# Performance work log

Hardware: AMD Instinct MI355X
Metric: run time of the kernel (lower is better)

Reference implementation:

```python
import jax, jax.numpy as jnp
import numpy as np

B, N, H, O = 262144, 64, 256, 64
MAX_ITER = 30
TOL = 1e-7
NU = 1.0


def setup_inputs() -> dict:
    key = jax.random.key(0)
    kx, kr, k1, k2, k3, k4 = jax.random.split(key, 6)
    x = jax.random.normal(kx, (B, N), dtype=jnp.float32) * 3.0
    r = jax.random.uniform(kr, (N,), dtype=jnp.float32) + 0.5  # positive rates in [0.5, 1.5)
    # MLP params (torch Linear: y = x @ W.T + b), Kaiming-ish scaling
    W1 = jax.random.normal(k1, (H, N), dtype=jnp.float32) * (1.0 / np.sqrt(N))
    b1 = jax.random.normal(k2, (H,), dtype=jnp.float32) * 0.01
    W2 = jax.random.normal(k3, (O, H), dtype=jnp.float32) * (1.0 / np.sqrt(H))
    b2 = jax.random.normal(k4, (O,), dtype=jnp.float32) * 0.01
    return {"x": x, "r": r, "W1": W1, "b1": b1, "W2": W2, "b2": b2}


def _solve_s(x, r):
    """Vectorized Newton solve of sum_i e^{-2 r_i s} x_i^2 = 1 per sample.

    Replicates solve_s_single: s starts at 0, up to MAX_ITER Newton steps,
    frozen once |F(s)| < TOL; all-zero samples return s = 0.
    """
    x2 = x * x  # [B, N]
    zero_mask = jnp.all(jnp.abs(x) <= 1e-12, axis=1)  # torch.allclose(x, 0, atol=1e-12)

    def body(_, s):
        e = jnp.exp(-2.0 * r[None, :] * s[:, None])        # [B, N]
        val = jnp.sum(e * x2, axis=1) - 1.0                # F(s)     [B]
        dval = jnp.sum(-2.0 * r[None, :] * e * x2, axis=1) # F'(s)    [B]
        safe_d = jnp.where(dval == 0.0, 1.0, dval)
        step = val / safe_d
        step = jnp.where((jnp.abs(val) < TOL) | zero_mask, 0.0, step)
        return s - step

    s0 = jnp.zeros(x.shape[0], dtype=x.dtype)
    return jax.lax.fori_loop(0, MAX_ITER, body, s0)


def reference(x, r, W1, b1, W2, b2):
    S = _solve_s(x, r)[:, None]                 # [B, 1], detached in torch (built via .item())
    S = jax.lax.stop_gradient(S)
    x_sphere = x * jnp.exp(-r[None, :] * S)     # d(-s) x
    h = jnp.maximum(x_sphere @ W1.T + b1, 0.0)  # [B, H]
    mlp_out = h @ W2.T + b2                     # [B, O]
    return mlp_out * jnp.exp(NU * S)
```

## Files before the change

### kernel.cpp

```cpp
#include <hip/hip_runtime.h>

typedef __attribute__((ext_vector_type(8))) short short8;
typedef __attribute__((ext_vector_type(4))) float floatx4;

static __device__ __forceinline__ unsigned short f2bf(float f) {
    unsigned u = __float_as_uint(f);
    u += 0x7FFFu + ((u >> 16) & 1u);
    return (unsigned short)(u >> 16);
}

__global__ __launch_bounds__(512, 2) void fused_k(const float* __restrict__ x,
                                                  const float* __restrict__ r,
                                                  const float* __restrict__ W1f,
                                                  const float* __restrict__ b1,
                                                  const float* __restrict__ W2f,
                                                  const float* __restrict__ b2,
                                                  float* __restrict__ out,
                                                  int tiles_per_block) {
    __shared__ unsigned short sW1[256 * 64];
    __shared__ unsigned short sW2[64 * 256];
    __shared__ unsigned short sH[128 * 32];

    int tid = threadIdx.x;

    const float4* w1f4 = (const float4*)W1f;
#pragma unroll
    for (int c = 0; c < 4; ++c) {
        int g = tid + c * 512;
        float4 lo = w1f4[2 * g], hi = w1f4[2 * g + 1];
        uint4 p;
        p.x = (unsigned)f2bf(lo.x) | ((unsigned)f2bf(lo.y) << 16);
        p.y = (unsigned)f2bf(lo.z) | ((unsigned)f2bf(lo.w) << 16);
        p.z = (unsigned)f2bf(hi.x) | ((unsigned)f2bf(hi.y) << 16);
        p.w = (unsigned)f2bf(hi.z) | ((unsigned)f2bf(hi.w) << 16);
        int row = g >> 3, ch = g & 7;
        *(uint4*)&sW1[row * 64 + (ch ^ (row & 7)) * 8] = p;
    }
    const float4* w2f4 = (const float4*)W2f;
#pragma unroll
    for (int c = 0; c < 4; ++c) {
        int g = tid + c * 512;
        float4 lo = w2f4[2 * g], hi = w2f4[2 * g + 1];
        uint4 p;
        p.x = (unsigned)f2bf(lo.x) | ((unsigned)f2bf(lo.y) << 16);
        p.y = (unsigned)f2bf(lo.z) | ((unsigned)f2bf(lo.w) << 16);
        p.z = (unsigned)f2bf(hi.x) | ((unsigned)f2bf(hi.y) << 16);
        p.w = (unsigned)f2bf(hi.z) | ((unsigned)f2bf(hi.w) << 16);
        int row = g >> 5, ch = g & 31;
        *(uint4*)&sW2[row * 256 + (ch ^ (row & 7)) * 8] = p;
    }
    __syncthreads();

    int wave = tid >> 6, lane = tid & 63;
    int q = lane >> 4, l16 = lane & 15;
    int sx = l16 & 7;

    float bias1[16];
#pragma unroll
    for (int n = 0; n < 16; ++n) bias1[n] = b1[n * 16 + l16];
    float bias2[4];
#pragma unroll
    for (int n = 0; n < 4; ++n) bias2[n] = b2[n * 16 + l16];

    const float L2E2 = 2.8853900817779268f;
    float rl2[16];
    {
        const float4* r4 = (const float4*)r;
        float4 ra = r4[2 * q], rb = r4[2 * q + 1];
        float4 rc = r4[8 + 2 * q], rd = r4[8 + 2 * q + 1];
        rl2[0] = ra.x * L2E2; rl2[1] = ra.y * L2E2; rl2[2] = ra.z * L2E2; rl2[3] = ra.w * L2E2;
        rl2[4] = rb.x * L2E2; rl2[5] = rb.y * L2E2; rl2[6] = rb.z * L2E2; rl2[7] = rb.w * L2E2;
        rl2[8] = rc.x * L2E2; rl2[9] = rc.y * L2E2; rl2[10] = rc.z * L2E2; rl2[11] = rc.w * L2E2;
        rl2[12] = rd.x * L2E2; rl2[13] = rd.y * L2E2; rl2[14] = rd.z * L2E2; rl2[15] = rd.w * L2E2;
    }

    for (int tt = 0; tt < tiles_per_block; ++tt) {
        size_t m0 = ((size_t)blockIdx.x * tiles_per_block + tt) * 128;
        int myrow = wave * 16 + l16;
        int rsw = myrow & 3;

        const float4* x4 = (const float4*)(x + (m0 + myrow) * 64);
        float4 va = x4[2 * q], vb = x4[2 * q + 1];
        float4 vc = x4[8 + 2 * q], vd = x4[8 + 2 * q + 1];
        float xv[16];
        xv[0] = va.x; xv[1] = va.y; xv[2] = va.z; xv[3] = va.w;
        xv[4] = vb.x; xv[5] = vb.y; xv[6] = vb.z; xv[7] = vb.w;
        xv[8] = vc.x; xv[9] = vc.y; xv[10] = vc.z; xv[11] = vc.w;
        xv[12] = vd.x; xv[13] = vd.y; xv[14] = vd.z; xv[15] = vd.w;

        float x2[16], rx2[16];
        float sum0 = 0.f, sumr = 0.f;
        int nz = 0;
#pragma unroll
        for (int j = 0; j < 16; ++j) {
            x2[j] = xv[j] * xv[j];
            rx2[j] = rl2[j] * x2[j];
            sum0 += x2[j];
            sumr += rx2[j];
            nz |= (fabsf(xv[j]) > 1e-12f) ? 1 : 0;
        }
        sum0 += __shfl_xor(sum0, 16); sum0 += __shfl_xor(sum0, 32);
        sumr += __shfl_xor(sumr, 16); sumr += __shfl_xor(sumr, 32);
        nz   |= __shfl_xor(nz, 16);   nz   |= __shfl_xor(nz, 32);

        float s = 0.f;
        if (nz) {
            s = __log2f(sum0) * sum0 * __builtin_amdgcn_rcpf(sumr);
#pragma unroll 1
            for (int it = 0; it < 10; ++it) {
                float ns = -s;
                float v = 0.f, dv = 0.f;
#pragma unroll
                for (int j = 0; j < 16; ++j) {
                    float e = __builtin_amdgcn_exp2f(ns * rl2[j]);
                    v = fmaf(e, x2[j], v);
                    dv = fmaf(e, rx2[j], dv);
                }
                v += __shfl_xor(v, 16);   v += __shfl_xor(v, 32);
                dv += __shfl_xor(dv, 16); dv += __shfl_xor(dv, 32);
                if (__all(fabsf(v - 1.f) < 1e-5f)) break;
                s += __log2f(v) * v * __builtin_amdgcn_rcpf(dv);
            }
        }

        float hs = -0.5f * s;
        short8 a0, a1;
#pragma unroll
        for (int j = 0; j < 8; ++j)
            a0[j] = (short)f2bf(xv[j] * __builtin_amdgcn_exp2f(hs * rl2[j]));
#pragma unroll
        for (int j = 0; j < 8; ++j)
            a1[j] = (short)f2bf(xv[8 + j] * __builtin_amdgcn_exp2f(hs * rl2[8 + j]));

        float es = __builtin_amdgcn_exp2f(s * 1.4426950408889634f);
        float sc[4];
#pragma unroll
        for (int reg = 0; reg < 4; ++reg) sc[reg] = __shfl(es, q * 4 + reg);

        floatx4 oacc[4];
#pragma unroll
        for (int n = 0; n < 4; ++n) oacc[n] = (floatx4){0.f, 0.f, 0.f, 0.f};

#pragma unroll
        for (int hc = 0; hc < 8; ++hc) {
#pragma unroll
            for (int n = 0; n < 2; ++n) {
                int hcol = hc * 2 + n;
                int row = hcol * 16 + l16;
                short8 wb0 = *(const short8*)&sW1[row * 64 + (q ^ sx) * 8];
                short8 wb1 = *(const short8*)&sW1[row * 64 + ((q + 4) ^ sx) * 8];
                floatx4 acc = {0.f, 0.f, 0.f, 0.f};
                acc = __builtin_amdgcn_mfma_f32_16x16x32_bf16(a0, wb0, acc, 0, 0, 0);
                acc = __builtin_amdgcn_mfma_f32_16x16x32_bf16(a1, wb1, acc, 0, 0, 0);
                float bias = bias1[hcol];
#pragma unroll
                for (int reg = 0; reg < 4; ++reg) {
                    float h = acc[reg] + bias;
                    h = h > 0.f ? h : 0.f;
                    int rr = wave * 16 + q * 4 + reg;
                    int E = n * 16 + l16;
                    sH[rr * 32 + (((E >> 3) ^ (rr & 3)) * 8) + (E & 7)] = f2bf(h);
                }
            }
            short8 ha = *(const short8*)&sH[myrow * 32 + ((q ^ rsw) * 8)];
#pragma unroll
            for (int n = 0; n < 4; ++n) {
                int row = n * 16 + l16;
                short8 wb = *(const short8*)&sW2[row * 256 + ((hc * 4 + q) ^ sx) * 8];
                oacc[n] = __builtin_amdgcn_mfma_f32_16x16x32_bf16(ha, wb, oacc[n], 0, 0, 0);
            }
        }
#pragma unroll
        for (int n = 0; n < 4; ++n) {
#pragma unroll
            for (int reg = 0; reg < 4; ++reg) {
                float o = (oacc[n][reg] + bias2[n]) * sc[reg];
                out[(m0 + wave * 16 + q * 4 + reg) * 64 + n * 16 + l16] = o;
            }
        }
    }
}

extern "C" void kernel_launch(void* const* d_in, const int* in_sizes, int n_in,
                              void* d_out, int out_size, void* d_ws, size_t ws_size,
                              hipStream_t stream) {
    const float* x  = (const float*)d_in[0];
    const float* r  = (const float*)d_in[1];
    const float* W1 = (const float*)d_in[2];
    const float* b1 = (const float*)d_in[3];
    const float* W2 = (const float*)d_in[4];
    const float* b2 = (const float*)d_in[5];
    float* out = (float*)d_out;
    int B = in_sizes[0] / 64;

    int tiles = B / 128;
    int blocks = 512;
    int tpb = tiles / blocks;

    fused_k<<<blocks, 512, 0, stream>>>(x, r, W1, b1, W2, b2, out, tpb);
}
```

Baseline: 146.4 us.

## Keep hidden activations in registers via transposed MFMA and permuted W1 rows

The first GEMM's operands are swapped (W1 as A, activations as B) and the W1 rows are permuted in LDS, so each lane's accumulator output lines up with the B-operand layout the second GEMM expects. The hidden activations are packed to bf16 in registers with v_cvt_pk_bf16_f32 instead of going through an LDS round trip. This removes the sH stores and loads along with their intra-wave dependency. Both biases are folded into the accumulator initial values (b1 is staged permuted in LDS), which drops the bias1 register array. The cost is index arithmetic that must match the MFMA lane layout exactly, so a mismatch would silently produce wrong results.

```diff
diff --git a/kernel.cpp b/kernel.cpp
--- a/kernel.cpp
+++ b/kernel.cpp
@@ -19,7 +19,7 @@
                                                   int tiles_per_block) {
     __shared__ unsigned short sW1[256 * 64];
     __shared__ unsigned short sW2[64 * 256];
-    __shared__ unsigned short sH[128 * 32];
+    __shared__ float sB1[256];
 
     int tid = threadIdx.x;
 
@@ -27,14 +27,15 @@
 #pragma unroll
     for (int c = 0; c < 4; ++c) {
         int g = tid + c * 512;
+        int h = g >> 3, ch = g & 7;
+        int prow = ((h >> 5) * 2 + ((h >> 2) & 1)) * 16 + ((h >> 3) & 3) * 4 + (h & 3);
         float4 lo = w1f4[2 * g], hi = w1f4[2 * g + 1];
         uint4 p;
         p.x = (unsigned)f2bf(lo.x) | ((unsigned)f2bf(lo.y) << 16);
         p.y = (unsigned)f2bf(lo.z) | ((unsigned)f2bf(lo.w) << 16);
         p.z = (unsigned)f2bf(hi.x) | ((unsigned)f2bf(hi.y) << 16);
         p.w = (unsigned)f2bf(hi.z) | ((unsigned)f2bf(hi.w) << 16);
-        int row = g >> 3, ch = g & 7;
-        *(uint4*)&sW1[row * 64 + (ch ^ (row & 7)) * 8] = p;
+        *(uint4*)&sW1[prow * 64 + (ch ^ (prow & 7)) * 8] = p;
     }
     const float4* w2f4 = (const float4*)W2f;
 #pragma unroll
@@ -49,15 +50,17 @@
         int row = g >> 5, ch = g & 31;
         *(uint4*)&sW2[row * 256 + (ch ^ (row & 7)) * 8] = p;
     }
+    if (tid < 256) {
+        int h = tid;
+        int prow = ((h >> 5) * 2 + ((h >> 2) & 1)) * 16 + ((h >> 3) & 3) * 4 + (h & 3);
+        sB1[prow] = b1[h];
+    }
     __syncthreads();
 
     int wave = tid >> 6, lane = tid & 63;
     int q = lane >> 4, l16 = lane & 15;
     int sx = l16 & 7;
 
-    float bias1[16];
-#pragma unroll
-    for (int n = 0; n < 16; ++n) bias1[n] = b1[n * 16 + l16];
     float bias2[4];
 #pragma unroll
     for (int n = 0; n < 4; ++n) bias2[n] = b2[n * 16 + l16];
@@ -77,7 +80,6 @@
     for (int tt = 0; tt < tiles_per_block; ++tt) {
         size_t m0 = ((size_t)blockIdx.x * tiles_per_block + tt) * 128;
         int myrow = wave * 16 + l16;
-        int rsw = myrow & 3;
 
         const float4* x4 = (const float4*)(x + (m0 + myrow) * 64);
         float4 va = x4[2 * q], vb = x4[2 * q + 1];
@@ -139,34 +141,46 @@
 
         floatx4 oacc[4];
 #pragma unroll
-        for (int n = 0; n < 4; ++n) oacc[n] = (floatx4){0.f, 0.f, 0.f, 0.f};
+        for (int n = 0; n < 4; ++n)
+            oacc[n] = (floatx4){bias2[n], bias2[n], bias2[n], bias2[n]};
 
 #pragma unroll
         for (int hc = 0; hc < 8; ++hc) {
-#pragma unroll
-            for (int n = 0; n < 2; ++n) {
-                int hcol = hc * 2 + n;
-                int row = hcol * 16 + l16;
+            unsigned pk0, pk1, pk2, pk3;
+            {
+                int t = hc * 2;
+                int row = t * 16 + l16;
                 short8 wb0 = *(const short8*)&sW1[row * 64 + (q ^ sx) * 8];
                 short8 wb1 = *(const short8*)&sW1[row * 64 + ((q + 4) ^ sx) * 8];
-                floatx4 acc = {0.f, 0.f, 0.f, 0.f};
-                acc = __builtin_amdgcn_mfma_f32_16x16x32_bf16(a0, wb0, acc, 0, 0, 0);
-                acc = __builtin_amdgcn_mfma_f32_16x16x32_bf16(a1, wb1, acc, 0, 0, 0);
-                float bias = bias1[hcol];
-#pragma unroll
-                for (int reg = 0; reg < 4; ++reg) {
-                    float h = acc[reg] + bias;
-                    h = h > 0.f ? h : 0.f;
-                    int rr = wave * 16 + q * 4 + reg;
-                    int E = n * 16 + l16;
-                    sH[rr * 32 + (((E >> 3) ^ (rr & 3)) * 8) + (E & 7)] = f2bf(h);
-                }
-            }
-            short8 ha = *(const short8*)&sH[myrow * 32 + ((q ^ rsw) * 8)];
+                const float4 bb = *(const float4*)&sB1[t * 16 + q * 4];
+                floatx4 acc = (floatx4){bb.x, bb.y, bb.z, bb.w};
+                acc = __builtin_amdgcn_mfma_f32_16x16x32_bf16(wb0, a0, acc, 0, 0, 0);
+                acc = __builtin_amdgcn_mfma_f32_16x16x32_bf16(wb1, a1, acc, 0, 0, 0);
+                float h0 = fmaxf(acc[0], 0.f), h1 = fmaxf(acc[1], 0.f);
+                float h2 = fmaxf(acc[2], 0.f), h3 = fmaxf(acc[3], 0.f);
+                asm("v_cvt_pk_bf16_f32 %0, %1, %2" : "=v"(pk0) : "v"(h0), "v"(h1));
+                asm("v_cvt_pk_bf16_f32 %0, %1, %2" : "=v"(pk1) : "v"(h2), "v"(h3));
+            }
+            {
+                int t = hc * 2 + 1;
+                int row = t * 16 + l16;
+                short8 wb0 = *(const short8*)&sW1[row * 64 + (q ^ sx) * 8];
+                short8 wb1 = *(const short8*)&sW1[row * 64 + ((q + 4) ^ sx) * 8];
+                const float4 bb = *(const float4*)&sB1[t * 16 + q * 4];
+                floatx4 acc = (floatx4){bb.x, bb.y, bb.z, bb.w};
+                acc = __builtin_amdgcn_mfma_f32_16x16x32_bf16(wb0, a0, acc, 0, 0, 0);
+                acc = __builtin_amdgcn_mfma_f32_16x16x32_bf16(wb1, a1, acc, 0, 0, 0);
+                float h0 = fmaxf(acc[0], 0.f), h1 = fmaxf(acc[1], 0.f);
+                float h2 = fmaxf(acc[2], 0.f), h3 = fmaxf(acc[3], 0.f);
+                asm("v_cvt_pk_bf16_f32 %0, %1, %2" : "=v"(pk2) : "v"(h0), "v"(h1));
+                asm("v_cvt_pk_bf16_f32 %0, %1, %2" : "=v"(pk3) : "v"(h2), "v"(h3));
+            }
+            int4 hw = make_int4((int)pk0, (int)pk1, (int)pk2, (int)pk3);
+            short8 ha = *(short8*)&hw;
 #pragma unroll
             for (int n = 0; n < 4; ++n) {
-                int row = n * 16 + l16;
-                short8 wb = *(const short8*)&sW2[row * 256 + ((hc * 4 + q) ^ sx) * 8];
+                int orow = n * 16 + l16;
+                short8 wb = *(const short8*)&sW2[orow * 256 + ((hc * 4 + q) ^ sx) * 8];
                 oacc[n] = __builtin_amdgcn_mfma_f32_16x16x32_bf16(ha, wb, oacc[n], 0, 0, 0);
             }
         }
@@ -174,8 +188,8 @@
         for (int n = 0; n < 4; ++n) {
 #pragma unroll
             for (int reg = 0; reg < 4; ++reg) {
-                float o = (oacc[n][reg] + bias2[n]) * sc[reg];
-                out[(m0 + wave * 16 + q * 4 + reg) * 64 + n * 16 + l16] = o;
+                out[(m0 + wave * 16 + q * 4 + reg) * 64 + n * 16 + l16] =
+                    oacc[n][reg] * sc[reg];
             }
         }
     }
```

Measured after the change: 139.0 us. 1.05x faster.
